# Kernel optimization log

Hardware: AMD Instinct MI355X
Metric: run time of the kernel (lower is better)

## Reference

```python
import jax, jax.numpy as jnp
import numpy as np

N_NODES = 8192
N_EDGES = 262144  # avg degree 32
F_IN = 128
F_OUT = 128


def setup_inputs() -> dict:
    key = jax.random.key(0)
    k1, k2, k3, k4 = jax.random.split(key, 4)
    x = jax.random.normal(k1, (N_NODES, F_IN), dtype=jnp.float32)
    edge_index = jax.random.randint(k2, (2, N_EDGES), 0, N_NODES, dtype=jnp.int32)
    # xavier_uniform-scale random W; B is a learned param (zeros at init, but
    # use random values so the x@B^T branch is exercised numerically)
    scale = np.float32(1.0 / np.sqrt(F_IN))
    W = jax.random.normal(k3, (F_OUT, F_IN), dtype=jnp.float32) * scale
    B = jax.random.normal(k4, (F_OUT, F_IN), dtype=jnp.float32) * scale
    return {"x": x, "edge_index": edge_index, "W": W, "B": B}


def reference(x, edge_index, W, B):
    num_nodes = x.shape[0]
    src, dst = edge_index[0], edge_index[1]
    # Dense adjacency: A[i, j] = 1 iff edge j -> i (duplicate edges collapse to 1,
    # matching torch's adj[dst, src] = 1.0 assignment semantics)
    A = jnp.zeros((num_nodes, num_nodes), dtype=jnp.float32).at[dst, src].set(1.0)
    # In-degree (counts duplicate edges, matching torch.bincount); degree-0 -> 1
    deg = jax.ops.segment_sum(jnp.ones_like(dst, dtype=jnp.float32), dst,
                              num_segments=num_nodes)
    deg = jnp.where(deg == 0, 1.0, deg)
    # D_inv @ A @ x @ W^T + x @ B^T; D_inv is diagonal -> row-scale by 1/deg
    msg = A @ (x @ W.T)           # [N, F_OUT]
    out = msg / deg[:, None] + x @ B.T
    return out
```

## Files before the change

### kernel.cpp

```cpp
#include <hip/hip_runtime.h>
#include <hip/hip_bf16.h>

constexpr int NN = 8192;
constexpr int NE = 262144;
constexpr int FD = 128;
constexpr int CAP = 64;

constexpr size_t H_OFF     = 0;
constexpr size_t H_BYTES   = (size_t)NN * FD * 2;
constexpr size_t CNT_OFF   = H_OFF + H_BYTES;
constexpr size_t CNT_BYTES = (size_t)NN * 4;
constexpr size_t COL_OFF   = CNT_OFF + CNT_BYTES;
constexpr size_t COL_BYTES = (size_t)NN * CAP * 4;
constexpr size_t XB_OFF    = COL_OFF + COL_BYTES;
constexpr size_t XB_BYTES  = (size_t)NN * FD * 2;
constexpr size_t UB_OFF    = XB_OFF + XB_BYTES;

typedef __attribute__((ext_vector_type(8))) short short8;
typedef __attribute__((ext_vector_type(4))) float f32x4;

__device__ __forceinline__ short f2b(float f) {
  union { __hip_bfloat16 b; short s; } u;
  u.b = __float2bfloat16(f);
  return u.s;
}

__global__ __launch_bounds__(256) void conv_kernel(
    const float* __restrict__ x, const float* __restrict__ W,
    const float* __restrict__ Bm, short* __restrict__ xb,
    short* __restrict__ ub, unsigned int* __restrict__ cnt) {
  const int t = blockIdx.x * 256 + threadIdx.x;

  const float4* xf4 = (const float4*)x;
  short4* xb4 = (short4*)xb;
#pragma unroll
  for (int j = 0; j < 4; ++j) {
    const int i = t + j * 65536;
    const float4 f = xf4[i];
    xb4[i] = short4{f2b(f.x), f2b(f.y), f2b(f.z), f2b(f.w)};
  }

  if (t < 2048) {
    const float4* src = (t < 1024) ? ((const float4*)W + t * 4)
                                   : ((const float4*)Bm + (t - 1024) * 4);
    short4* dst = (short4*)ub + t * 4;
#pragma unroll
    for (int j = 0; j < 4; ++j) {
      const float4 f = src[j];
      dst[j] = short4{f2b(f.x), f2b(f.y), f2b(f.z), f2b(f.w)};
    }
    ((uint4*)cnt)[t] = uint4{0u, 0u, 0u, 0u};
  }
}

__global__ __launch_bounds__(256) void fillgemm_kernel(
    const int* __restrict__ ei, unsigned int* __restrict__ cnt,
    int* __restrict__ col, const short* __restrict__ xb,
    const short* __restrict__ ub, __hip_bfloat16* __restrict__ h,
    float* __restrict__ out) {
  const int tid = threadIdx.x;

  if (blockIdx.x < 256) {
    const int e = (blockIdx.x * 256 + tid) * 4;
    const int4 s4 = *(const int4*)(ei + e);
    const int4 d4 = *(const int4*)(ei + NE + e);
#pragma unroll
    for (int r = 0; r < 4; ++r) {
      const int src = (&s4.x)[r];
      const int dst = (&d4.x)[r];
      const unsigned int pos = atomicAdd(&cnt[dst], 1u);
      if (pos < CAP) col[(size_t)dst * CAP + pos] = src;
    }
    return;
  }

  const int gid = blockIdx.x - 256;
  const int bm = (gid >> 2) * 128;
  const int bn = (gid & 3) * 64;
  const int w = tid >> 6;
  const int lane = tid & 63;
  const int l15 = lane & 15;
  const int l4 = lane >> 4;
  const int row0 = bm + w * 32;

  f32x4 acc[2][4] = {};

#pragma unroll
  for (int kk = 0; kk < 4; ++kk) {
    const int koff = kk * 32 + l4 * 8;
    const short8 a0 = *(const short8*)(xb + (size_t)(row0 + l15) * FD + koff);
    const short8 a1 = *(const short8*)(xb + (size_t)(row0 + 16 + l15) * FD + koff);
#pragma unroll
    for (int ni = 0; ni < 4; ++ni) {
      const short8 b = *(const short8*)(ub + (size_t)(bn + ni * 16 + l15) * FD + koff);
      acc[0][ni] = __builtin_amdgcn_mfma_f32_16x16x32_bf16(a0, b, acc[0][ni], 0, 0, 0);
      acc[1][ni] = __builtin_amdgcn_mfma_f32_16x16x32_bf16(a1, b, acc[1][ni], 0, 0, 0);
    }
  }

#pragma unroll
  for (int mi = 0; mi < 2; ++mi) {
#pragma unroll
    for (int ni = 0; ni < 4; ++ni) {
      const int n = bn + ni * 16 + l15;
#pragma unroll
      for (int r = 0; r < 4; ++r) {
        const int row = row0 + mi * 16 + l4 * 4 + r;
        const float v = acc[mi][ni][r];
        if (n < FD) h[(size_t)row * FD + n] = __float2bfloat16(v);
        else        out[(size_t)row * FD + (n - FD)] = v;
      }
    }
  }
}

__global__ __launch_bounds__(256) void gather_kernel(
    const unsigned int* __restrict__ h,
    const int* __restrict__ col, const unsigned int* __restrict__ cnt,
    float* __restrict__ out) {
  __shared__ unsigned int bmp[4][NN / 32];

  const int w    = threadIdx.x >> 6;
  const int lane = threadIdx.x & 63;
  const int node = blockIdx.x * 4 + w;
  const int c  = lane & 15;
  const int eu = lane >> 4;
  const unsigned int n = cnt[node];
  const unsigned int nn = (n < (unsigned)CAP) ? n : (unsigned)CAP;
  const int* cl = col + (size_t)node * CAP;

  const int colv = cl[lane];

  ((uint4*)bmp[w])[lane] = uint4{0u, 0u, 0u, 0u};
  __syncthreads();

  int keep = colv;
  if (lane < (int)nn) {
    const unsigned int mask = 1u << (colv & 31);
    const unsigned int old = atomicOr(&bmp[w][colv >> 5], mask);
    if (old & mask) keep = -1;
  }

  float acc[8];
#pragma unroll
  for (int i = 0; i < 8; ++i) acc[i] = 0.f;

  for (unsigned int base = 0; base < nn; base += 4) {
    const unsigned int e = base + eu;
    const int s = __shfl(keep, (int)e, 64);
    if (e < nn && s >= 0) {
      const uint4 v = *(const uint4*)(h + (size_t)s * (FD / 2) + (c << 2));
      acc[0] += __uint_as_float(v.x << 16);
      acc[1] += __uint_as_float(v.x & 0xffff0000u);
      acc[2] += __uint_as_float(v.y << 16);
      acc[3] += __uint_as_float(v.y & 0xffff0000u);
      acc[4] += __uint_as_float(v.z << 16);
      acc[5] += __uint_as_float(v.z & 0xffff0000u);
      acc[6] += __uint_as_float(v.w << 16);
      acc[7] += __uint_as_float(v.w & 0xffff0000u);
    }
  }

#pragma unroll
  for (int i = 0; i < 8; ++i) {
    acc[i] += __shfl_xor(acc[i], 16, 64);
    acc[i] += __shfl_xor(acc[i], 32, 64);
  }

  if (eu == 0) {
    const float r = 1.0f / (n ? (float)n : 1.0f);
    float* op = out + (size_t)node * FD + c * 8;
    float4 o0 = *(float4*)op;
    float4 o1 = *(float4*)(op + 4);
    o0.x += acc[0] * r; o0.y += acc[1] * r; o0.z += acc[2] * r; o0.w += acc[3] * r;
    o1.x += acc[4] * r; o1.y += acc[5] * r; o1.z += acc[6] * r; o1.w += acc[7] * r;
    *(float4*)op = o0;
    *(float4*)(op + 4) = o1;
  }
}

extern "C" void kernel_launch(void* const* d_in, const int* in_sizes, int n_in,
                              void* d_out, int out_size, void* d_ws, size_t ws_size,
                              hipStream_t stream) {
  const float* x  = (const float*)d_in[0];
  const int* ei   = (const int*)d_in[1];
  const float* W  = (const float*)d_in[2];
  const float* Bm = (const float*)d_in[3];
  float* out = (float*)d_out;

  char* ws = (char*)d_ws;
  __hip_bfloat16* h = (__hip_bfloat16*)(ws + H_OFF);
  unsigned int* cnt = (unsigned int*)(ws + CNT_OFF);
  int* col          = (int*)(ws + COL_OFF);
  short* xb         = (short*)(ws + XB_OFF);
  short* ub         = (short*)(ws + UB_OFF);

  conv_kernel<<<256, 256, 0, stream>>>(x, W, Bm, xb, ub, cnt);
  fillgemm_kernel<<<512, 256, 0, stream>>>(ei, cnt, col, xb, ub, h, out);
  gather_kernel<<<NN / 4, 256, 0, stream>>>((const unsigned int*)h, col, cnt, out);
}
```

Baseline: 36.10 us.

## Fuse x bf16 conversion into GEMM and retile to full-N per wave

```diff
diff --git a/kernel.cpp b/kernel.cpp
--- a/kernel.cpp
+++ b/kernel.cpp
@@ -12,9 +12,7 @@
 constexpr size_t CNT_BYTES = (size_t)NN * 4;
 constexpr size_t COL_OFF   = CNT_OFF + CNT_BYTES;
 constexpr size_t COL_BYTES = (size_t)NN * CAP * 4;
-constexpr size_t XB_OFF    = COL_OFF + COL_BYTES;
-constexpr size_t XB_BYTES  = (size_t)NN * FD * 2;
-constexpr size_t UB_OFF    = XB_OFF + XB_BYTES;
+constexpr size_t UB_OFF    = COL_OFF + COL_BYTES;
 
 typedef __attribute__((ext_vector_type(8))) short short8;
 typedef __attribute__((ext_vector_type(4))) float f32x4;
@@ -25,37 +23,18 @@
   return u.s;
 }
 
-__global__ __launch_bounds__(256) void conv_kernel(
-    const float* __restrict__ x, const float* __restrict__ W,
-    const float* __restrict__ Bm, short* __restrict__ xb,
+__global__ __launch_bounds__(256) void prep_kernel(
+    const float* __restrict__ W, const float* __restrict__ Bm,
     short* __restrict__ ub, unsigned int* __restrict__ cnt) {
   const int t = blockIdx.x * 256 + threadIdx.x;
-
-  const float4* xf4 = (const float4*)x;
-  short4* xb4 = (short4*)xb;
-#pragma unroll
-  for (int j = 0; j < 4; ++j) {
-    const int i = t + j * 65536;
-    const float4 f = xf4[i];
-    xb4[i] = short4{f2b(f.x), f2b(f.y), f2b(f.z), f2b(f.w)};
-  }
-
-  if (t < 2048) {
-    const float4* src = (t < 1024) ? ((const float4*)W + t * 4)
-                                   : ((const float4*)Bm + (t - 1024) * 4);
-    short4* dst = (short4*)ub + t * 4;
-#pragma unroll
-    for (int j = 0; j < 4; ++j) {
-      const float4 f = src[j];
-      dst[j] = short4{f2b(f.x), f2b(f.y), f2b(f.z), f2b(f.w)};
-    }
-    ((uint4*)cnt)[t] = uint4{0u, 0u, 0u, 0u};
-  }
+  const float4 f = (t < 4096) ? ((const float4*)W)[t] : ((const float4*)Bm)[t - 4096];
+  ((short4*)ub)[t] = short4{f2b(f.x), f2b(f.y), f2b(f.z), f2b(f.w)};
+  if (t < 2048) ((uint4*)cnt)[t] = uint4{0u, 0u, 0u, 0u};
 }
 
 __global__ __launch_bounds__(256) void fillgemm_kernel(
     const int* __restrict__ ei, unsigned int* __restrict__ cnt,
-    int* __restrict__ col, const short* __restrict__ xb,
+    int* __restrict__ col, const float* __restrict__ x,
     const short* __restrict__ ub, __hip_bfloat16* __restrict__ h,
     float* __restrict__ out) {
   const int tid = threadIdx.x;
@@ -75,41 +54,38 @@
   }
 
   const int gid = blockIdx.x - 256;
-  const int bm = (gid >> 2) * 128;
-  const int bn = (gid & 3) * 64;
   const int w = tid >> 6;
   const int lane = tid & 63;
   const int l15 = lane & 15;
   const int l4 = lane >> 4;
-  const int row0 = bm + w * 32;
+  const int row0 = gid * 64 + w * 16;
 
-  f32x4 acc[2][4] = {};
+  f32x4 acc[16] = {};
 
 #pragma unroll
   for (int kk = 0; kk < 4; ++kk) {
     const int koff = kk * 32 + l4 * 8;
-    const short8 a0 = *(const short8*)(xb + (size_t)(row0 + l15) * FD + koff);
-    const short8 a1 = *(const short8*)(xb + (size_t)(row0 + 16 + l15) * FD + koff);
+    const float4* xp = (const float4*)(x + (size_t)(row0 + l15) * FD + koff);
+    const float4 f0 = xp[0];
+    const float4 f1 = xp[1];
+    const short8 a = short8{f2b(f0.x), f2b(f0.y), f2b(f0.z), f2b(f0.w),
+                            f2b(f1.x), f2b(f1.y), f2b(f1.z), f2b(f1.w)};
 #pragma unroll
-    for (int ni = 0; ni < 4; ++ni) {
-      const short8 b = *(const short8*)(ub + (size_t)(bn + ni * 16 + l15) * FD + koff);
-      acc[0][ni] = __builtin_amdgcn_mfma_f32_16x16x32_bf16(a0, b, acc[0][ni], 0, 0, 0);
-      acc[1][ni] = __builtin_amdgcn_mfma_f32_16x16x32_bf16(a1, b, acc[1][ni], 0, 0, 0);
+    for (int ni = 0; ni < 16; ++ni) {
+      const short8 b = *(const short8*)(ub + (size_t)(ni * 16 + l15) * FD + koff);
+      acc[ni] = __builtin_amdgcn_mfma_f32_16x16x32_bf16(a, b, acc[ni], 0, 0, 0);
     }
   }
 
 #pragma unroll
-  for (int mi = 0; mi < 2; ++mi) {
+  for (int ni = 0; ni < 16; ++ni) {
+    const int n = ni * 16 + l15;
 #pragma unroll
-    for (int ni = 0; ni < 4; ++ni) {
-      const int n = bn + ni * 16 + l15;
-#pragma unroll
-      for (int r = 0; r < 4; ++r) {
-        const int row = row0 + mi * 16 + l4 * 4 + r;
-        const float v = acc[mi][ni][r];
-        if (n < FD) h[(size_t)row * FD + n] = __float2bfloat16(v);
-        else        out[(size_t)row * FD + (n - FD)] = v;
-      }
+    for (int r = 0; r < 4; ++r) {
+      const int row = row0 + l4 * 4 + r;
+      const float v = acc[ni][r];
+      if (n < FD) h[(size_t)row * FD + n] = __float2bfloat16(v);
+      else        out[(size_t)row * FD + (n - FD)] = v;
     }
   }
 }
@@ -192,10 +168,9 @@
   __hip_bfloat16* h = (__hip_bfloat16*)(ws + H_OFF);
   unsigned int* cnt = (unsigned int*)(ws + CNT_OFF);
   int* col          = (int*)(ws + COL_OFF);
-  short* xb         = (short*)(ws + XB_OFF);
   short* ub         = (short*)(ws + UB_OFF);
 
-  conv_kernel<<<256, 256, 0, stream>>>(x, W, Bm, xb, ub, cnt);
-  fillgemm_kernel<<<512, 256, 0, stream>>>(ei, cnt, col, xb, ub, h, out);
+  prep_kernel<<<32, 256, 0, stream>>>(W, Bm, ub, cnt);
+  fillgemm_kernel<<<384, 256, 0, stream>>>(ei, cnt, col, x, ub, h, out);
   gather_kernel<<<NN / 4, 256, 0, stream>>>((const unsigned int*)h, col, cnt, out);
 }
```

Result: slower. 44.70 us (+23.8%).
